# Kernel optimization log

Measured on AMD Instinct MI355X. Metric: run time of the kernel, lower is better.

## Reference

```python
import jax, jax.numpy as jnp
import numpy as np

N = 100000          # nodes
E = 1600000         # edges (avg degree 16)
H = 128             # hidden_dim
P = 10              # INVARIANT_PHYSICS_DIM
TOTAL = P + H
LN_EPS = 1e-5       # torch LayerNorm default


def setup_inputs() -> dict:
    key = jax.random.key(0)
    ks = jax.random.split(key, 16)
    s = 0.02
    return {
        "physics_x": jax.random.normal(ks[0], (N, P), dtype=jnp.float32),
        "learnable_emb": jax.random.normal(ks[1], (N, H), dtype=jnp.float32),
        "edge_index": jax.random.randint(ks[2], (2, E), 0, N, dtype=jnp.int32),
        "Wq": jax.random.normal(ks[3], (TOTAL, H), dtype=jnp.float32) * s,
        "bq": jnp.zeros((H,), dtype=jnp.float32),
        "Wk": jax.random.normal(ks[4], (TOTAL, H), dtype=jnp.float32) * s,
        "bk": jnp.zeros((H,), dtype=jnp.float32),
        "Wv": jax.random.normal(ks[5], (H, H), dtype=jnp.float32) * s,
        "bv": jnp.zeros((H,), dtype=jnp.float32),
        "Wo": jax.random.normal(ks[6], (H, H), dtype=jnp.float32) * s,
        "bo": jnp.zeros((H,), dtype=jnp.float32),
        "gamma": jnp.ones((H,), dtype=jnp.float32),
        "beta": jnp.zeros((H,), dtype=jnp.float32),
    }


def reference(physics_x, learnable_emb, edge_index, Wq, bq, Wk, bk, Wv, bv, Wo, bo, gamma, beta):
    n_nodes = learnable_emb.shape[0]
    scale = 1.0 / np.sqrt(Wq.shape[1]).astype(np.float32)

    full_repr = jnp.concatenate([physics_x, learnable_emb], axis=-1)   # [N, P+H]
    Q = full_repr @ Wq + bq                                            # [N, H]
    K = full_repr @ Wk + bk                                            # [N, H]
    V = learnable_emb @ Wv + bv                                        # [N, H]

    src, dst = edge_index[0], edge_index[1]
    # per-edge unnormalized attention (NOTE: no max-subtraction, faithful to source)
    attn_scores = jnp.sum(Q[dst] * K[src], axis=-1) * scale            # [E]
    exp_scores = jnp.exp(attn_scores)                                  # [E]
    denom = jax.ops.segment_sum(exp_scores, dst, num_segments=n_nodes) # [N]
    attn_probs = exp_scores / (denom[dst] + 1e-8)                      # [E]

    msg = V[src] * attn_probs[:, None]                                 # [E, H]
    agg = jax.ops.segment_sum(msg, dst, num_segments=n_nodes)          # [N, H]

    out = agg @ Wo + bo
    x = learnable_emb + out
    mu = jnp.mean(x, axis=-1, keepdims=True)
    var = jnp.var(x, axis=-1, keepdims=True)
    return gamma * (x - mu) / jnp.sqrt(var + LN_EPS) + beta
```

## Files before the change

### kernel.cpp

```cpp
#include <hip/hip_runtime.h>
#include <hip/hip_bf16.h>
#include <math.h>

#define PDIM 10
#define HDIM 128
#define TDIM 138
#define AROW 168
#define AROW2 136
#define B_LEN (5 * 8 * 64 * 8)
#define TROW 136

#define CW_WQ 0
#define CW_WK 17664
#define CW_WV 35328
#define CW_WO 51712
#define CW_BQ 68096
#define CW_BK 68224
#define CW_BV 68352
#define CW_BO 68480
#define CW_GA 68608
#define CW_BE 68736
#define CW_TOTAL 68864

typedef short v8s __attribute__((ext_vector_type(8)));
typedef float v4f __attribute__((ext_vector_type(4)));
typedef float v2f __attribute__((ext_vector_type(2)));

#if defined(__has_builtin)
#if __has_builtin(__builtin_amdgcn_cvt_pk_f32_fp8) && __has_builtin(__builtin_amdgcn_cvt_pk_fp8_f32)
#define HAVE_FP8_CVT 1
#endif
#endif
#ifndef HAVE_FP8_CVT
#define HAVE_FP8_CVT 0
#endif

#if HAVE_FP8_CVT
#define DEC_EXTRA 1.0f
#else
#define DEC_EXTRA 0x1p120f
#endif

__device__ __forceinline__ float b2f_lo(unsigned u) { return __uint_as_float(u << 16); }
__device__ __forceinline__ float b2f_hi(unsigned u) { return __uint_as_float(u & 0xffff0000u); }
__device__ __forceinline__ unsigned short f2b(float f) {
    unsigned u = __float_as_uint(f);
    u += 0x7fffu + ((u >> 16) & 1u);
    return (unsigned short)(u >> 16);
}

__device__ __forceinline__ float f8_raw(unsigned t) {
    unsigned bits = ((t & 0x80u) << 24) | ((t & 0x7fu) << 20);
    return __uint_as_float(bits);
}
__device__ __forceinline__ unsigned f8_enc1(float f) {
    unsigned u = __float_as_uint(f);
    unsigned s = (u >> 31) << 7;
    float a = fabsf(f);
    if (a < 0.0009765625f) return s;
    if (a < 0.015625f) {
        int m = (int)(a * 512.f + 0.5f); if (m > 7) m = 7;
        return s | (unsigned)m;
    }
    if (a >= 448.f) return s | 0x7e;
    int ex = (int)((u >> 23) & 0xff);
    unsigned mant = u & 0x7fffff;
    unsigned r = mant >> 20, rem = mant & 0xfffff;
    if (rem > 0x80000u || (rem == 0x80000u && (r & 1))) r++;
    if (r == 8) { r = 0; ex++; }
    if (ex - 127 > 8) return s | 0x7e;
    return s | (unsigned)((ex - 120) << 3) | r;
}

__device__ __forceinline__ void dot4x(unsigned w, const float* q, float& p) {
#if HAVE_FP8_CVT
    v2f lo = __builtin_amdgcn_cvt_pk_f32_fp8((int)w, false);
    v2f hi = __builtin_amdgcn_cvt_pk_f32_fp8((int)w, true);
    p = fmaf(q[0], lo[0], p); p = fmaf(q[1], lo[1], p);
    p = fmaf(q[2], hi[0], p); p = fmaf(q[3], hi[1], p);
#else
    p = fmaf(q[0], f8_raw(w), p);
    p = fmaf(q[1], f8_raw(w >> 8), p);
    p = fmaf(q[2], f8_raw(w >> 16), p);
    p = fmaf(q[3], f8_raw(w >> 24), p);
#endif
}
__device__ __forceinline__ void acc4x(unsigned w, float e, float* acc) {
#if HAVE_FP8_CVT
    v2f lo = __builtin_amdgcn_cvt_pk_f32_fp8((int)w, false);
    v2f hi = __builtin_amdgcn_cvt_pk_f32_fp8((int)w, true);
    acc[0] = fmaf(e, lo[0], acc[0]); acc[1] = fmaf(e, lo[1], acc[1]);
    acc[2] = fmaf(e, hi[0], acc[2]); acc[3] = fmaf(e, hi[1], acc[3]);
#else
    acc[0] = fmaf(e, f8_raw(w), acc[0]);
    acc[1] = fmaf(e, f8_raw(w >> 8), acc[1]);
    acc[2] = fmaf(e, f8_raw(w >> 16), acc[2]);
    acc[3] = fmaf(e, f8_raw(w >> 24), acc[3]);
#endif
}
__device__ __forceinline__ uint2 pack8(uint4 t) {
#if HAVE_FP8_CVT
    int u0 = __builtin_amdgcn_cvt_pk_fp8_f32(b2f_lo(t.x), b2f_hi(t.x), 0, false);
    u0 = __builtin_amdgcn_cvt_pk_fp8_f32(b2f_lo(t.y), b2f_hi(t.y), u0, true);
    int u1 = __builtin_amdgcn_cvt_pk_fp8_f32(b2f_lo(t.z), b2f_hi(t.z), 0, false);
    u1 = __builtin_amdgcn_cvt_pk_fp8_f32(b2f_lo(t.w), b2f_hi(t.w), u1, true);
    return make_uint2((unsigned)u0, (unsigned)u1);
#else
    unsigned u0 = f8_enc1(b2f_lo(t.x)) | (f8_enc1(b2f_hi(t.x)) << 8)
                | (f8_enc1(b2f_lo(t.y)) << 16) | (f8_enc1(b2f_hi(t.y)) << 24);
    unsigned u1 = f8_enc1(b2f_lo(t.z)) | (f8_enc1(b2f_hi(t.z)) << 8)
                | (f8_enc1(b2f_lo(t.w)) << 16) | (f8_enc1(b2f_hi(t.w)) << 24);
    return make_uint2(u0, u1);
#endif
}

__global__ void ws_sentinel_kernel(float* out, int bucket)
{
    if (threadIdx.x == 0) out[0] = ldexpf(1.f + (float)bucket / 256.f, 100);
}

__global__ __launch_bounds__(256) void convert_weights(
    const float* Wq, const float* Wk, const float* Wv, const float* Wo,
    const float* bq, const float* bk, const float* bv, const float* bo,
    const float* ga, const float* be,
    float* __restrict__ dst)
{
    int idx = blockIdx.x * 256 + threadIdx.x;
    if (idx >= CW_TOTAL) return;
    const float* src; int loc;
    if      (idx < CW_WK) { src = Wq; loc = idx - CW_WQ; }
    else if (idx < CW_WV) { src = Wk; loc = idx - CW_WK; }
    else if (idx < CW_WO) { src = Wv; loc = idx - CW_WV; }
    else if (idx < CW_BQ) { src = Wo; loc = idx - CW_WO; }
    else if (idx < CW_BK) { src = bq; loc = idx - CW_BQ; }
    else if (idx < CW_BV) { src = bk; loc = idx - CW_BK; }
    else if (idx < CW_BO) { src = bv; loc = idx - CW_BV; }
    else if (idx < CW_GA) { src = bo; loc = idx - CW_BO; }
    else if (idx < CW_BE) { src = ga; loc = idx - CW_GA; }
    else                  { src = be; loc = idx - CW_BE; }
    dst[idx] = src[loc];
}

__global__ __launch_bounds__(256) void pack_wfrag(
    const float* __restrict__ cw, unsigned short* __restrict__ wfrag)
{
    int g = blockIdx.x * 256 + threadIdx.x;
    if (g >= 4 * 5 * 8 * 64) return;
    int lane = g & 63;
    int nt   = (g >> 6) & 7;
    int mk   = g >> 9;
    int kc = mk % 5, mat = mk / 5;
    int quad = lane >> 4, l15 = lane & 15;
    int n = nt * 16 + l15;

    unsigned short* dst = wfrag + (size_t)g * 8;
    #pragma unroll
    for (int j = 0; j < 8; ++j) {
        int k = kc * 32 + quad * 8 + j;
        float v = 0.f;
        if (mat == 0)      { if (k < TDIM) v = cw[CW_WQ + k * HDIM + n]; }
        else if (mat == 1) { if (k < TDIM) v = cw[CW_WK + k * HDIM + n]; }
        else if (mat == 2) { if (k >= PDIM && k < TDIM) v = cw[CW_WV + (k - PDIM) * HDIM + n]; }
        else               { if (k < HDIM) v = cw[CW_WO + k * HDIM + n]; }
        dst[j] = f2b(v);
    }
}

__global__ __launch_bounds__(256, 5) void qkv_mfma_kernel(
    const float* __restrict__ physics, const float* __restrict__ emb,
    const float* __restrict__ cw, const unsigned short* __restrict__ wfrag,
    unsigned short* __restrict__ Qb, unsigned char* __restrict__ K8,
    unsigned char* __restrict__ V8, int n_nodes)
{
    __shared__ __align__(16) unsigned short smem[64 * AROW];

    const int tid = threadIdx.x;
    const int nbase = blockIdx.x * 64;
    const int lane = tid & 63;
    const int w = tid >> 6;
    const int quad = lane >> 4;
    const int l15 = lane & 15;

    for (int idx = tid; idx < 64 * 5; idx += 256) {
        int r = idx / 5, p = idx - r * 5;
        int node = nbase + r;
        float v0 = 0.f, v1 = 0.f;
        if (node < n_nodes) {
            const float* ph = physics + (size_t)node * PDIM + 2 * p;
            v0 = ph[0]; v1 = ph[1];
        }
        ((unsigned*)smem)[r * 84 + p] = (unsigned)f2b(v0) | ((unsigned)f2b(v1) << 16);
    }
    for (int idx = tid; idx < 64 * 32; idx += 256) {
        int r = idx >> 5, c = idx & 31;
        int node = nbase + r;
        float4 e = make_float4(0.f, 0.f, 0.f, 0.f);
        if (node < n_nodes) e = *(const float4*)(emb + (size_t)node * HDIM + 4 * c);
        unsigned* dst = (unsigned*)smem + r * 84 + 5 + 2 * c;
        dst[0] = (unsigned)f2b(e.x) | ((unsigned)f2b(e.y) << 16);
        dst[1] = (unsigned)f2b(e.z) | ((unsigned)f2b(e.w) << 16);
    }
    for (int idx = tid; idx < 64 * 15; idx += 256) {
        int r = idx / 15, p = idx - r * 15;
        ((unsigned*)smem)[r * 84 + 69 + p] = 0;
    }
    __syncthreads();

    v8s a_frag[5];
    #pragma unroll
    for (int kc = 0; kc < 5; ++kc)
        a_frag[kc] = *(v8s*)(smem + (w * 16 + l15) * AROW + kc * 32 + quad * 8);
    __syncthreads();

    const int r_out = tid >> 2;
    const int cseg = (tid & 3) * 32;
    const int node_out = nbase + r_out;

    for (int mat = 0; mat < 3; ++mat) {
        const v8s* bglob = (const v8s*)(wfrag + (size_t)mat * B_LEN) + lane;

        v4f acc[8];
        #pragma unroll
        for (int nt = 0; nt < 8; ++nt) acc[nt] = (v4f){0.f, 0.f, 0.f, 0.f};

        #pragma unroll
        for (int kc = 0; kc < 5; ++kc) {
            #pragma unroll
            for (int nt = 0; nt < 8; ++nt) {
                v8s b = bglob[(kc * 8 + nt) * 64];
                acc[nt] = __builtin_amdgcn_mfma_f32_16x16x32_bf16(
                    a_frag[kc], b, acc[nt], 0, 0, 0);
            }
        }

        #pragma unroll
        for (int nt = 0; nt < 8; ++nt) {
            float bias = cw[CW_BQ + mat * HDIM + nt * 16 + l15];
            #pragma unroll
            for (int reg = 0; reg < 4; ++reg) {
                int row = w * 16 + quad * 4 + reg;
                smem[row * TROW + nt * 16 + l15] = f2b(acc[nt][reg] + bias);
            }
        }
        __syncthreads();

        if (node_out < n_nodes) {
            const unsigned short* srcp = smem + r_out * TROW + cseg;
            if (mat == 0) {
                unsigned short* dst = Qb + (size_t)node_out * HDIM + cseg;
                #pragma unroll
                for (int j = 0; j < 4; ++j)
                    ((uint4*)dst)[j] = *(const uint4*)(srcp + 8 * j);
            } else {
                unsigned char* dst8 = (mat == 1 ? K8 : V8) + (size_t)node_out * HDIM + cseg;
                uint4 t0 = *(const uint4*)(srcp);
                uint4 t1 = *(const uint4*)(srcp + 8);
                uint4 t2 = *(const uint4*)(srcp + 16);
                uint4 t3 = *(const uint4*)(srcp + 24);
                uint2 p0 = pack8(t0), p1 = pack8(t1), p2 = pack8(t2), p3 = pack8(t3);
                ((uint4*)dst8)[0] = make_uint4(p0.x, p0.y, p1.x, p1.y);
                ((uint4*)dst8)[1] = make_uint4(p2.x, p2.y, p3.x, p3.y);
            }
        }
        if (mat < 2) __syncthreads();
    }
}

#define FILL_NPART 8
#define FILL_CHUNKS 512
__global__ __launch_bounds__(256) void degree_part_kernel(
    const int* __restrict__ ei, int* __restrict__ deg, int n_edges, int n_nodes)
{
    const int part = blockIdx.x & (FILL_NPART - 1);
    const int chunk = blockIdx.x >> 3;
    const int W = (n_nodes + FILL_NPART - 1) / FILL_NPART;
    const int lo = part * W;
    const int hi = min(n_nodes, lo + W);
    const int epc = (n_edges + FILL_CHUNKS - 1) / FILL_CHUNKS;
    const int e0 = chunk * epc;
    const int e1 = min(n_edges, e0 + epc);

    for (int e = e0 + (int)threadIdx.x; e < e1; e += 256) {
        int d = ei[n_edges + e];
        d = max(0, min(d, n_nodes - 1));
        if (d >= lo && d < hi) atomicAdd(&deg[d], 1);
    }
}

__global__ __launch_bounds__(256) void scan_bsum(
    const int* __restrict__ deg, int* __restrict__ bsum, int n)
{
    __shared__ int s[256];
    int i = blockIdx.x * 256 + threadIdx.x;
    s[threadIdx.x] = (i < n) ? deg[i] : 0;
    __syncthreads();
    for (int off = 128; off > 0; off >>= 1) {
        if (threadIdx.x < off) s[threadIdx.x] += s[threadIdx.x + off];
        __syncthreads();
    }
    if (threadIdx.x == 0) bsum[blockIdx.x] = s[0];
}

__global__ __launch_bounds__(512) void scan_boff(
    const int* __restrict__ bsum, int* __restrict__ boff, int nb)
{
    __shared__ int s[512];
    int t = threadIdx.x;
    int v = (t < nb) ? bsum[t] : 0;
    s[t] = v;
    __syncthreads();
    for (int off = 1; off < 512; off <<= 1) {
        int u = (t >= off) ? s[t - off] : 0;
        __syncthreads();
        s[t] += u;
        __syncthreads();
    }
    if (t < nb) boff[t] = s[t] - v;
}

__global__ __launch_bounds__(256) void scan_final(
    const int* __restrict__ deg, const int* __restrict__ boff,
    int* __restrict__ row_off, int n)
{
    __shared__ int s[256];
    int t = threadIdx.x;
    int i = blockIdx.x * 256 + t;
    int v = (i < n) ? deg[i] : 0;
    s[t] = v;
    __syncthreads();
    for (int off = 1; off < 256; off <<= 1) {
        int u = (t >= off) ? s[t - off] : 0;
        __syncthreads();
        s[t] += u;
        __syncthreads();
    }
    int base = boff[blockIdx.x];
    if (i < n) row_off[i] = base + s[t] - v;
    if (i == n - 1) row_off[n] = base + s[t];
}

__global__ __launch_bounds__(256) void fill_part_kernel(
    const int* __restrict__ ei, const int* __restrict__ row_off,
    int* __restrict__ cursor, int* __restrict__ csr_src, int n_edges, int n_nodes)
{
    const int part = blockIdx.x & (FILL_NPART - 1);
    const int chunk = blockIdx.x >> 3;
    const int W = (n_nodes + FILL_NPART - 1) / FILL_NPART;
    const int lo = part * W;
    const int hi = min(n_nodes, lo + W);
    const int epc = (n_edges + FILL_CHUNKS - 1) / FILL_CHUNKS;
    const int e0 = chunk * epc;
    const int e1 = min(n_edges, e0 + epc);

    for (int e = e0 + (int)threadIdx.x; e < e1; e += 256) {
        int d = ei[n_edges + e];
        d = max(0, min(d, n_nodes - 1));
        if (d >= lo && d < hi) {
            int pos = atomicAdd(&cursor[d], 1);
            csr_src[row_off[d] + pos] = ei[e];
        }
    }
}

__global__ __launch_bounds__(256) void attn_fused_kernel(
    const unsigned short* __restrict__ Qb, const unsigned char* __restrict__ K8,
    const unsigned char* __restrict__ V8,
    const int* __restrict__ row_off, const int* __restrict__ csr_src,
    unsigned short* __restrict__ aggb, int n_nodes, int n_edges)
{
    const int wid = (int)((blockIdx.x * 256 + threadIdx.x) >> 6);
    const int lane = threadIdx.x & 63;
    if (wid >= n_nodes) return;
    const int eg = lane >> 3;
    const int cg = lane & 7;

    const float qscale = 0.088388347648318447f * DEC_EXTRA;
    const uint4* qp = (const uint4*)(Qb + (size_t)wid * HDIM + cg * 16);
    uint4 qa = qp[0], qb = qp[1];
    float q[16];
    q[0]  = b2f_lo(qa.x) * qscale; q[1]  = b2f_hi(qa.x) * qscale;
    q[2]  = b2f_lo(qa.y) * qscale; q[3]  = b2f_hi(qa.y) * qscale;
    q[4]  = b2f_lo(qa.z) * qscale; q[5]  = b2f_hi(qa.z) * qscale;
    q[6]  = b2f_lo(qa.w) * qscale; q[7]  = b2f_hi(qa.w) * qscale;
    q[8]  = b2f_lo(qb.x) * qscale; q[9]  = b2f_hi(qb.x) * qscale;
    q[10] = b2f_lo(qb.y) * qscale; q[11] = b2f_hi(qb.y) * qscale;
    q[12] = b2f_lo(qb.z) * qscale; q[13] = b2f_hi(qb.z) * qscale;
    q[14] = b2f_lo(qb.w) * qscale; q[15] = b2f_hi(qb.w) * qscale;

    int beg = row_off[wid], end = row_off[wid + 1];
    beg = max(0, min(beg, n_edges));
    end = max(beg, min(end, n_edges));

    float acc[16];
    #pragma unroll
    for (int j = 0; j < 16; ++j) acc[j] = 0.f;
    float den = 0.f;

    for (int i = beg; i < end; i += 8) {
        int idx = i + eg;
        bool valid = idx < end;
        int s = csr_src[valid ? idx : (end - 1)];
        s = max(0, min(s, n_nodes - 1));
        uint4 kr = *(const uint4*)(K8 + (size_t)s * HDIM + cg * 16);
        uint4 vr = *(const uint4*)(V8 + (size_t)s * HDIM + cg * 16);

        float p = 0.f;
        dot4x(kr.x, q + 0, p);
        dot4x(kr.y, q + 4, p);
        dot4x(kr.z, q + 8, p);
        dot4x(kr.w, q + 12, p);
        p += __shfl_xor(p, 1);
        p += __shfl_xor(p, 2);
        p += __shfl_xor(p, 4);

        float e = valid ? __expf(fminf(p, 60.f)) : 0.f;
        den += e;
        acc4x(vr.x, e, acc + 0);
        acc4x(vr.y, e, acc + 4);
        acc4x(vr.z, e, acc + 8);
        acc4x(vr.w, e, acc + 12);
    }

    #pragma unroll
    for (int j = 0; j < 16; ++j) {
        acc[j] += __shfl_xor(acc[j], 8);
        acc[j] += __shfl_xor(acc[j], 16);
        acc[j] += __shfl_xor(acc[j], 32);
    }
    den += __shfl_xor(den, 8);
    den += __shfl_xor(den, 16);
    den += __shfl_xor(den, 32);

    float inv = 1.f / (den + 1e-8f);
    if (eg == 0) {
        unsigned* dst = (unsigned*)(aggb + (size_t)wid * HDIM + cg * 16);
        #pragma unroll
        for (int j = 0; j < 8; ++j) {
            float a0 = (acc[2*j]     * DEC_EXTRA) * inv;
            float a1 = (acc[2*j + 1] * DEC_EXTRA) * inv;
            dst[j] = (unsigned)f2b(a0) | ((unsigned)f2b(a1) << 16);
        }
    }
}

__global__ __launch_bounds__(256) void out_ln_mfma_kernel(
    const unsigned short* __restrict__ aggb, const float* __restrict__ emb,
    const float* __restrict__ cw, const unsigned short* __restrict__ wfrag,
    float* __restrict__ out, int n_nodes)
{
    __shared__ __align__(16) unsigned short smem[64 * AROW2];
    const int tid = threadIdx.x;
    const int nbase = blockIdx.x * 64;
    const int lane = tid & 63;
    const int w = tid >> 6;
    const int quad = lane >> 4;
    const int l15 = lane & 15;

    for (int idx = tid; idx < 64 * 16; idx += 256) {
        int r = idx >> 4, c = idx & 15;
        int node = nbase + r;
        uint4 v = make_uint4(0u, 0u, 0u, 0u);
        if (node < n_nodes) v = ((const uint4*)(aggb + (size_t)node * HDIM))[c];
        *(uint4*)((char*)smem + r * (AROW2 * 2) + c * 16) = v;
    }
    __syncthreads();

    v8s a_frag[4];
    #pragma unroll
    for (int kc = 0; kc < 4; ++kc)
        a_frag[kc] = *(v8s*)(smem + (w * 16 + l15) * AROW2 + kc * 32 + quad * 8);

    const v8s* bglob = (const v8s*)(wfrag + (size_t)3 * B_LEN) + lane;
    v4f acc[8];
    #pragma unroll
    for (int nt = 0; nt < 8; ++nt) acc[nt] = (v4f){0.f, 0.f, 0.f, 0.f};

    #pragma unroll
    for (int kc = 0; kc < 4; ++kc) {
        #pragma unroll
        for (int nt = 0; nt < 8; ++nt) {
            v8s b = bglob[(kc * 8 + nt) * 64];
            acc[nt] = __builtin_amdgcn_mfma_f32_16x16x32_bf16(
                a_frag[kc], b, acc[nt], 0, 0, 0);
        }
    }

    const int row = w * 16 + quad * 4;
    #pragma unroll
    for (int nt = 0; nt < 8; ++nt) {
        int col = nt * 16 + l15;
        float bo_v = cw[CW_BO + col];
        #pragma unroll
        for (int reg = 0; reg < 4; ++reg) {
            int node = nbase + row + reg;
            float e = (node < n_nodes) ? emb[(size_t)node * HDIM + col] : 0.f;
            acc[nt][reg] += bo_v + e;
        }
    }

    float s1[4] = {0.f, 0.f, 0.f, 0.f};
    float s2[4] = {0.f, 0.f, 0.f, 0.f};
    #pragma unroll
    for (int nt = 0; nt < 8; ++nt)
        #pragma unroll
        for (int reg = 0; reg < 4; ++reg) {
            s1[reg] += acc[nt][reg];
            s2[reg] = fmaf(acc[nt][reg], acc[nt][reg], s2[reg]);
        }
    #pragma unroll
    for (int mask = 1; mask <= 8; mask <<= 1) {
        #pragma unroll
        for (int reg = 0; reg < 4; ++reg) {
            s1[reg] += __shfl_xor(s1[reg], mask);
            s2[reg] += __shfl_xor(s2[reg], mask);
        }
    }
    float mu[4], rs[4];
    #pragma unroll
    for (int reg = 0; reg < 4; ++reg) {
        mu[reg] = s1[reg] * (1.f / 128.f);
        float var = fmaxf(s2[reg] * (1.f / 128.f) - mu[reg] * mu[reg], 0.f);
        rs[reg] = rsqrtf(var + 1e-5f);
    }

    #pragma unroll
    for (int nt = 0; nt < 8; ++nt) {
        int col = nt * 16 + l15;
        float ga_v = cw[CW_GA + col];
        float be_v = cw[CW_BE + col];
        #pragma unroll
        for (int reg = 0; reg < 4; ++reg) {
            int node = nbase + row + reg;
            if (node < n_nodes)
                out[(size_t)node * HDIM + col] =
                    ga_v * (acc[nt][reg] - mu[reg]) * rs[reg] + be_v;
        }
    }
}

extern "C" void kernel_launch(void* const* d_in, const int* in_sizes, int n_in,
                              void* d_out, int out_size, void* d_ws, size_t ws_size,
                              hipStream_t stream)
{
    const float* physics = (const float*)d_in[0];
    const float* emb     = (const float*)d_in[1];
    const int*   ei      = (const int*)d_in[2];

    const int n_nodes = in_sizes[1] / HDIM;
    const int n_edges = in_sizes[2] / 2;
    const int NB = (n_nodes + 255) / 256;

    char* ws = (char*)d_ws;
    size_t off = 0;
    auto alloc = [&](size_t bytes) -> void* {
        void* p = ws + off;
        off = (off + bytes + 255) & ~(size_t)255;
        return p;
    };

    float* cw      = (float*)alloc((size_t)CW_TOTAL * 4);
    unsigned short* wfrag = (unsigned short*)alloc((size_t)4 * B_LEN * 2);
    int* deg       = (int*)alloc((size_t)2 * n_nodes * 4);
    int* cursor    = deg + n_nodes;
    int* row_off   = (int*)alloc((size_t)(n_nodes + 1) * 4);
    int* bsum      = (int*)alloc((size_t)NB * 4);
    int* boff      = (int*)alloc((size_t)NB * 4);
    int* csr_src   = (int*)alloc((size_t)n_edges * 4);
    unsigned short* Qb = (unsigned short*)alloc((size_t)n_nodes * HDIM * 2);
    unsigned char* K8  = (unsigned char*)alloc((size_t)n_nodes * HDIM);
    unsigned char* V8  = (unsigned char*)alloc((size_t)n_nodes * HDIM);
    unsigned short* aggb = (unsigned short*)alloc((size_t)n_nodes * HDIM * 2);

    if (ws_size < off) {
        int bucket = (int)min((size_t)255, ws_size >> 24);
        ws_sentinel_kernel<<<1, 64, 0, stream>>>((float*)d_out, bucket);
        return;
    }

    hipMemsetAsync(deg, 0, (size_t)2 * n_nodes * sizeof(int), stream);

    convert_weights<<<(CW_TOTAL + 255) / 256, 256, 0, stream>>>(
        (const float*)d_in[3], (const float*)d_in[5], (const float*)d_in[7],
        (const float*)d_in[9], (const float*)d_in[4], (const float*)d_in[6],
        (const float*)d_in[8], (const float*)d_in[10], (const float*)d_in[11],
        (const float*)d_in[12], cw);

    pack_wfrag<<<(4 * 5 * 8 * 64 + 255) / 256, 256, 0, stream>>>(cw, wfrag);
    qkv_mfma_kernel<<<(n_nodes + 63) / 64, 256, 0, stream>>>(
        physics, emb, cw, wfrag, Qb, K8, V8, n_nodes);

    degree_part_kernel<<<FILL_NPART * FILL_CHUNKS, 256, 0, stream>>>(
        ei, deg, n_edges, n_nodes);
    scan_bsum<<<NB, 256, 0, stream>>>(deg, bsum, n_nodes);
    scan_boff<<<1, 512, 0, stream>>>(bsum, boff, NB);
    scan_final<<<NB, 256, 0, stream>>>(deg, boff, row_off, n_nodes);
    fill_part_kernel<<<FILL_NPART * FILL_CHUNKS, 256, 0, stream>>>(
        ei, row_off, cursor, csr_src, n_edges, n_nodes);

    attn_fused_kernel<<<(n_nodes + 3) / 4, 256, 0, stream>>>(
        Qb, K8, V8, row_off, csr_src, aggb, n_nodes, n_edges);

    out_ln_mfma_kernel<<<(n_nodes + 63) / 64, 256, 0, stream>>>(
        aggb, emb, cw, wfrag, (float*)d_out, n_nodes);
}
```

Measured before the change: 430.7 us.

## Fuse CSR construction into a single cooperative kernel with grid syncs

Replaces the memset, degree count, three-stage scan and fill launches with one cooperative kernel of 384 blocks that uses grid.sync between phases. It also switches the scan to 512-node chunks with a single-block offset scan. The aim is to remove launch overhead and the inter-kernel gaps among the small CSR-building steps. In exchange, far fewer blocks do the edge passes (384 instead of 4096), and each grid-wide barrier has its own cost, so the atomic-heavy phases may lose parallelism.

```diff
diff --git a/kernel.cpp b/kernel.cpp
--- a/kernel.cpp
+++ b/kernel.cpp
@@ -1,6 +1,9 @@
 #include <hip/hip_runtime.h>
 #include <hip/hip_bf16.h>
+#include <hip/hip_cooperative_groups.h>
 #include <math.h>
+
+namespace cg = cooperative_groups;
 
 #define PDIM 10
 #define HDIM 128
@@ -266,93 +269,89 @@
     }
 }
 
-#define FILL_NPART 8
-#define FILL_CHUNKS 512
-__global__ __launch_bounds__(256) void degree_part_kernel(
-    const int* __restrict__ ei, int* __restrict__ deg, int n_edges, int n_nodes)
-{
-    const int part = blockIdx.x & (FILL_NPART - 1);
-    const int chunk = blockIdx.x >> 3;
-    const int W = (n_nodes + FILL_NPART - 1) / FILL_NPART;
+#define CSR_BLOCKS 384
+#define CSR_NPART 8
+#define CSR_NCHG (CSR_BLOCKS / CSR_NPART)
+#define CSR_CHUNK 512
+
+__global__ __launch_bounds__(256) void csr_coop_kernel(
+    const int* __restrict__ ei, int* __restrict__ deg, int* __restrict__ cursor,
+    int* __restrict__ row_off, int* __restrict__ bsum, int* __restrict__ boff,
+    int* __restrict__ csr_src, int n_edges, int n_nodes)
+{
+    cg::grid_group grid = cg::this_grid();
+    __shared__ int s[CSR_CHUNK];
+    __shared__ int t[256];
+
+    const int tid = (int)threadIdx.x;
+    const int gid = (int)blockIdx.x * 256 + tid;
+    const int gsz = CSR_BLOCKS * 256;
+
+    const int part = (int)blockIdx.x & (CSR_NPART - 1);
+    const int pchunk = (int)blockIdx.x >> 3;
+    const int W = (n_nodes + CSR_NPART - 1) / CSR_NPART;
     const int lo = part * W;
     const int hi = min(n_nodes, lo + W);
-    const int epc = (n_edges + FILL_CHUNKS - 1) / FILL_CHUNKS;
-    const int e0 = chunk * epc;
+    const int epc = (n_edges + CSR_NCHG - 1) / CSR_NCHG;
+    const int e0 = pchunk * epc;
     const int e1 = min(n_edges, e0 + epc);
 
-    for (int e = e0 + (int)threadIdx.x; e < e1; e += 256) {
+    for (int i = gid; i < 2 * n_nodes; i += gsz) deg[i] = 0;
+    grid.sync();
+
+    for (int e = e0 + tid; e < e1; e += 256) {
         int d = ei[n_edges + e];
         d = max(0, min(d, n_nodes - 1));
         if (d >= lo && d < hi) atomicAdd(&deg[d], 1);
     }
-}
-
-__global__ __launch_bounds__(256) void scan_bsum(
-    const int* __restrict__ deg, int* __restrict__ bsum, int n)
-{
-    __shared__ int s[256];
-    int i = blockIdx.x * 256 + threadIdx.x;
-    s[threadIdx.x] = (i < n) ? deg[i] : 0;
-    __syncthreads();
-    for (int off = 128; off > 0; off >>= 1) {
-        if (threadIdx.x < off) s[threadIdx.x] += s[threadIdx.x + off];
+    grid.sync();
+
+    const int nchunks = (n_nodes + CSR_CHUNK - 1) / CSR_CHUNK;
+    for (int c = (int)blockIdx.x; c < nchunks; c += CSR_BLOCKS) {
+        int base = c * CSR_CHUNK;
+        for (int j = tid; j < CSR_CHUNK; j += 256) {
+            int i = base + j;
+            s[j] = (i < n_nodes) ? deg[i] : 0;
+        }
         __syncthreads();
-    }
-    if (threadIdx.x == 0) bsum[blockIdx.x] = s[0];
-}
-
-__global__ __launch_bounds__(512) void scan_boff(
-    const int* __restrict__ bsum, int* __restrict__ boff, int nb)
-{
-    __shared__ int s[512];
-    int t = threadIdx.x;
-    int v = (t < nb) ? bsum[t] : 0;
-    s[t] = v;
-    __syncthreads();
-    for (int off = 1; off < 512; off <<= 1) {
-        int u = (t >= off) ? s[t - off] : 0;
+        for (int off = 1; off < CSR_CHUNK; off <<= 1) {
+            int j0 = tid, j1 = tid + 256;
+            int v0 = (j0 >= off) ? s[j0 - off] : 0;
+            int v1 = (j1 >= off) ? s[j1 - off] : 0;
+            __syncthreads();
+            s[j0] += v0;
+            s[j1] += v1;
+            __syncthreads();
+        }
+        for (int j = tid; j < CSR_CHUNK; j += 256) {
+            int i = base + j;
+            if (i < n_nodes) row_off[i] = (j == 0) ? 0 : s[j - 1];
+        }
+        if (tid == 0) bsum[c] = s[CSR_CHUNK - 1];
         __syncthreads();
-        s[t] += u;
+    }
+    grid.sync();
+
+    if (blockIdx.x == 0) {
+        int v = (tid < nchunks) ? bsum[tid] : 0;
+        t[tid] = v;
         __syncthreads();
-    }
-    if (t < nb) boff[t] = s[t] - v;
-}
-
-__global__ __launch_bounds__(256) void scan_final(
-    const int* __restrict__ deg, const int* __restrict__ boff,
-    int* __restrict__ row_off, int n)
-{
-    __shared__ int s[256];
-    int t = threadIdx.x;
-    int i = blockIdx.x * 256 + t;
-    int v = (i < n) ? deg[i] : 0;
-    s[t] = v;
-    __syncthreads();
-    for (int off = 1; off < 256; off <<= 1) {
-        int u = (t >= off) ? s[t - off] : 0;
-        __syncthreads();
-        s[t] += u;
-        __syncthreads();
-    }
-    int base = boff[blockIdx.x];
-    if (i < n) row_off[i] = base + s[t] - v;
-    if (i == n - 1) row_off[n] = base + s[t];
-}
-
-__global__ __launch_bounds__(256) void fill_part_kernel(
-    const int* __restrict__ ei, const int* __restrict__ row_off,
-    int* __restrict__ cursor, int* __restrict__ csr_src, int n_edges, int n_nodes)
-{
-    const int part = blockIdx.x & (FILL_NPART - 1);
-    const int chunk = blockIdx.x >> 3;
-    const int W = (n_nodes + FILL_NPART - 1) / FILL_NPART;
-    const int lo = part * W;
-    const int hi = min(n_nodes, lo + W);
-    const int epc = (n_edges + FILL_CHUNKS - 1) / FILL_CHUNKS;
-    const int e0 = chunk * epc;
-    const int e1 = min(n_edges, e0 + epc);
-
-    for (int e = e0 + (int)threadIdx.x; e < e1; e += 256) {
+        for (int off = 1; off < 256; off <<= 1) {
+            int u = (tid >= off) ? t[tid - off] : 0;
+            __syncthreads();
+            t[tid] += u;
+            __syncthreads();
+        }
+        if (tid < nchunks) boff[tid] = t[tid] - v;
+    }
+    grid.sync();
+
+    for (int i = gid; i < n_nodes; i += gsz)
+        row_off[i] += boff[i / CSR_CHUNK];
+    if (gid == 0) row_off[n_nodes] = n_edges;
+    grid.sync();
+
+    for (int e = e0 + tid; e < e1; e += 256) {
         int d = ei[n_edges + e];
         d = max(0, min(d, n_nodes - 1));
         if (d >= lo && d < hi) {
@@ -577,8 +576,6 @@
         return;
     }
 
-    hipMemsetAsync(deg, 0, (size_t)2 * n_nodes * sizeof(int), stream);
-
     convert_weights<<<(CW_TOTAL + 255) / 256, 256, 0, stream>>>(
         (const float*)d_in[3], (const float*)d_in[5], (const float*)d_in[7],
         (const float*)d_in[9], (const float*)d_in[4], (const float*)d_in[6],
@@ -589,13 +586,17 @@
     qkv_mfma_kernel<<<(n_nodes + 63) / 64, 256, 0, stream>>>(
         physics, emb, cw, wfrag, Qb, K8, V8, n_nodes);
 
-    degree_part_kernel<<<FILL_NPART * FILL_CHUNKS, 256, 0, stream>>>(
-        ei, deg, n_edges, n_nodes);
-    scan_bsum<<<NB, 256, 0, stream>>>(deg, bsum, n_nodes);
-    scan_boff<<<1, 512, 0, stream>>>(bsum, boff, NB);
-    scan_final<<<NB, 256, 0, stream>>>(deg, boff, row_off, n_nodes);
-    fill_part_kernel<<<FILL_NPART * FILL_CHUNKS, 256, 0, stream>>>(
-        ei, row_off, cursor, csr_src, n_edges, n_nodes);
+    {
+        const int* ei_a = ei;
+        int* deg_a = deg; int* cur_a = cursor; int* ro_a = row_off;
+        int* bs_a = bsum; int* bo_a = boff; int* cs_a = csr_src;
+        int ne_a = n_edges; int nn_a = n_nodes;
+        void* args[] = { (void*)&ei_a, (void*)&deg_a, (void*)&cur_a,
+                         (void*)&ro_a, (void*)&bs_a, (void*)&bo_a,
+                         (void*)&cs_a, (void*)&ne_a, (void*)&nn_a };
+        hipLaunchCooperativeKernel((const void*)csr_coop_kernel,
+                                   dim3(CSR_BLOCKS), dim3(256), args, 0, stream);
+    }
 
     attn_fused_kernel<<<(n_nodes + 3) / 4, 256, 0, stream>>>(
         Qb, K8, V8, row_off, csr_src, aggb, n_nodes, n_edges);
```

Result: slower. 719.6 us (+67.1%).
